# Kernel tuning notes

Measured on AMD Instinct MI355X. Metric: run time of the kernel, lower is better.

Reference implementation:

```python
import jax, jax.numpy as jnp
import numpy as np

N_LEVELS = 1024
K = 8  # number of spike timesteps; d/T have length K+1 (index 0 unused)
X_SHAPE = (64, 512, 1024)


def setup_inputs() -> dict:
    key = jax.random.key(0)
    kx, kh0, kh, kd, kT = jax.random.split(key, 5)
    x = jax.random.normal(kx, X_SHAPE, dtype=jnp.float32) * 2.0
    # h: [N_LEVELS, K+1]; column 0 is the sorted search grid (required by searchsorted)
    h0 = jnp.sort(jax.random.uniform(kh0, (N_LEVELS,), minval=-4.0, maxval=4.0))
    h = jax.random.normal(kh, (N_LEVELS, K + 1), dtype=jnp.float32)
    h = h.at[:, 0].set(h0)
    d = jax.random.uniform(kd, (K + 1,), minval=0.05, maxval=1.0)
    T = jax.random.uniform(kT, (K + 1,), minval=-1.0, maxval=1.0)
    b = jnp.float32(0.1)
    return {"x": x, "h": h, "d": d, "T": T, "b": b}


def reference(x, h, d, T, b):
    sp = x.shape
    xf = x.reshape(-1)
    grid = h[:, 0]  # sorted lookup grid
    n = grid.shape[0]
    idx = jnp.clip(jnp.searchsorted(grid, xf), 1, n - 1)
    left = grid[idx - 1]
    right = grid[idx]
    take_left = jnp.abs(xf - left) < jnp.abs(xf - right)
    nearest = jnp.where(take_left, left, right)          # quantized input
    nidx = jnp.where(take_left, idx - 1, idx)            # per-element row into h
    kmax = d.shape[0] - 1
    v = nearest
    out = jnp.zeros_like(xf)
    # loop over the small fixed number of thresholds (data dims fully vectorized)
    for t in range(1, kmax + 1):
        z = (v - T[t] >= 0).astype(xf.dtype)
        out = out + z * d[t]
        if t != kmax:
            v = h[nidx, t + 1]  # irregular per-element gather
    out = out - b
    return out.reshape(sp)
```

## Files before the change

kernel.cpp:

```cpp
#include <hip/hip_runtime.h>
#include <math.h>

#define NL  1024
#define KP1 9
#define NB  8192

#define WS_TAB 4
#define WS_BS  1028
#define WS_BKT 2060

__device__ __forceinline__ unsigned oi(float f) {
    unsigned u = __float_as_uint(f);
    return (u & 0x80000000u) ? ~u : (u | 0x80000000u);
}
__device__ __forceinline__ float unoi(unsigned k) {
    return __uint_as_float((k & 0x80000000u) ? (k & 0x7fffffffu) : ~k);
}

__device__ __forceinline__ int bidx(float x, float lo0, float inv) {
    float t = (x - lo0) * inv;
    int j = (int)t;
    j = j < 0 ? 0 : j;
    j = j > (NB - 1) ? (NB - 1) : j;
    return j;
}

__global__ __launch_bounds__(1024) void build_kernel(
    const float* __restrict__ h, const float* __restrict__ d,
    const float* __restrict__ T, const float* __restrict__ bp,
    float* __restrict__ ws)
{
    __shared__ float s_g[NL];
    __shared__ float s_B[NL];
    __shared__ int   s_jb[NL];
    __shared__ float s_lo0, s_inv;

    const int tid = threadIdx.x;
    float g = h[tid * KP1];
    s_g[tid] = g;

    {
        float v = g, outv = 0.0f, b = bp[0];
#pragma unroll
        for (int t = 1; t <= 8; ++t) {
            float z = ((v - T[t]) >= 0.0f) ? 1.0f : 0.0f;
            outv = outv + z * d[t];
            if (t != 8) v = h[tid * KP1 + (t + 1)];
        }
        ws[WS_TAB + tid] = outv - b;
    }
    __syncthreads();

    if (tid < NL - 1) {
        float l = s_g[tid], r = s_g[tid + 1];
        unsigned a = oi(l), b2 = oi(r);
        while (a < b2) {
            unsigned m = a + ((b2 - a) >> 1);
            float xm = unoi(m);
            float dl = fabsf(xm - l), dr = fabsf(xm - r);
            if (!(dl < dr)) b2 = m; else a = m + 1;
        }
        s_B[tid] = unoi(a);
    } else {
        s_B[tid] = INFINITY;
    }
    __syncthreads();

    if (tid == 0) {
        float lo0 = s_B[0];
        float inv = (float)NB / (s_B[NL - 2] - lo0);
        s_lo0 = lo0; s_inv = inv;
        ws[0] = lo0; ws[1] = inv;
    }
    __syncthreads();

    float lo0 = s_lo0, inv = s_inv;
    s_jb[tid] = (tid < NL - 1) ? bidx(s_B[tid], lo0, inv) : 0x7fffffff;
    ws[WS_BS + tid] = s_B[tid];
    if (tid < 8) ws[WS_BS + NL + tid] = INFINITY;
    __syncthreads();

    unsigned short* bucket = (unsigned short*)(ws + WS_BKT);
    for (int j = tid; j < NB; j += 1024) {
        int lo = 0;
#pragma unroll
        for (int s = 512; s >= 1; s >>= 1)
            if (s_jb[lo + s - 1] < j) lo += s;
        bucket[j] = (unsigned short)lo;
    }
}

__global__ __launch_bounds__(256) void ps_act_kernel(
    const float* __restrict__ x,
    const float* __restrict__ ws,
    float* __restrict__ out,
    int n4)
{
    __shared__ float          stab[NL];
    __shared__ float          sBs[NL + 8];
    __shared__ unsigned short sbk[NB];

    const int tid = threadIdx.x;
    for (int i = tid; i < NL; i += 256)     stab[i] = ws[WS_TAB + i];
    for (int i = tid; i < NL + 8; i += 256) sBs[i]  = ws[WS_BS + i];
    const unsigned short* gbk = (const unsigned short*)(ws + WS_BKT);
    for (int i = tid; i < NB; i += 256)     sbk[i]  = gbk[i];
    const float lo0 = ws[0];
    const float inv = ws[1];
    __syncthreads();

    const float4* __restrict__ x4 = (const float4*)x;
    float4* __restrict__ o4 = (float4*)out;
    const int stride = gridDim.x * blockDim.x;

    for (int i4 = blockIdx.x * blockDim.x + tid; i4 < n4; i4 += stride) {
        float4 xv = x4[i4];
        float xin[4] = {xv.x, xv.y, xv.z, xv.w};
        float xo[4];
#pragma unroll
        for (int e = 0; e < 4; ++e) {
            float xf = xin[e];
            int j = bidx(xf, lo0, inv);
            int ni = sbk[j];
            while (sBs[ni] <= xf) ++ni;
            xo[e] = stab[ni];
        }
        o4[i4] = make_float4(xo[0], xo[1], xo[2], xo[3]);
    }
}

extern "C" void kernel_launch(void* const* d_in, const int* in_sizes, int n_in,
                              void* d_out, int out_size, void* d_ws, size_t ws_size,
                              hipStream_t stream) {
    const float* x = (const float*)d_in[0];
    const float* h = (const float*)d_in[1];
    const float* d = (const float*)d_in[2];
    const float* T = (const float*)d_in[3];
    const float* b = (const float*)d_in[4];
    float* out = (float*)d_out;
    float* ws  = (float*)d_ws;

    int n  = in_sizes[0];
    int n4 = n / 4;

    build_kernel<<<1, 1024, 0, stream>>>(h, d, T, b, ws);
    ps_act_kernel<<<4096, 256, 0, stream>>>(x, ws, out, n4);
}
```

Measured before the change: 253.8 us.

## Replace bucket index plus linear scan with per-bucket resolved lookup records

The bucket table now stores a float4 record per bucket holding the single boundary and the left and right output values, so most elements resolve with one LDS read and one compare. Buckets with two or more boundaries fall back to a linear scan over global memory. Bucket count drops to 2048 so the records fit in LDS. Loads and stores become nontemporal and the grid shrinks to 1024 blocks. Trade-off: coarser buckets may send more elements down the slower global fallback path, which also diverges.

```diff
diff --git a/kernel.cpp b/kernel.cpp
--- a/kernel.cpp
+++ b/kernel.cpp
@@ -3,11 +3,13 @@
 
 #define NL  1024
 #define KP1 9
-#define NB  8192
+#define NB  2048
 
 #define WS_TAB 4
 #define WS_BS  1028
-#define WS_BKT 2060
+#define WS_REC 2064
+
+typedef float f32x4 __attribute__((ext_vector_type(4)));
 
 __device__ __forceinline__ unsigned oi(float f) {
     unsigned u = __float_as_uint(f);
@@ -32,6 +34,7 @@
 {
     __shared__ float s_g[NL];
     __shared__ float s_B[NL];
+    __shared__ float s_tab[NL];
     __shared__ int   s_jb[NL];
     __shared__ float s_lo0, s_inv;
 
@@ -47,7 +50,9 @@
             outv = outv + z * d[t];
             if (t != 8) v = h[tid * KP1 + (t + 1)];
         }
-        ws[WS_TAB + tid] = outv - b;
+        float tv = outv - b;
+        s_tab[tid] = tv;
+        ws[WS_TAB + tid] = tv;
     }
     __syncthreads();
 
@@ -80,13 +85,22 @@
     if (tid < 8) ws[WS_BS + NL + tid] = INFINITY;
     __syncthreads();
 
-    unsigned short* bucket = (unsigned short*)(ws + WS_BKT);
+    float4* rec = (float4*)(ws + WS_REC);
     for (int j = tid; j < NB; j += 1024) {
-        int lo = 0;
+        int s0 = 0, s1 = 0;
 #pragma unroll
         for (int s = 512; s >= 1; s >>= 1)
-            if (s_jb[lo + s - 1] < j) lo += s;
-        bucket[j] = (unsigned short)lo;
+            if (s_jb[s0 + s - 1] < j) s0 += s;
+#pragma unroll
+        for (int s = 512; s >= 1; s >>= 1)
+            if (s_jb[s1 + s - 1] < j + 1) s1 += s;
+        int cnt = s1 - s0;
+        float S, vL, vR; unsigned aux = 0u;
+        if (cnt == 0)      { S = INFINITY; vL = s_tab[s0]; vR = vL; }
+        else if (cnt == 1) { S = s_B[s0];  vL = s_tab[s0]; vR = s_tab[s0 + 1]; }
+        else               { S = 0.0f; vL = 0.0f; vR = 0.0f;
+                             aux = 0x80000000u | (unsigned)s0; }
+        rec[j] = make_float4(S, vL, vR, __uint_as_float(aux));
     }
 }
 
@@ -96,36 +110,40 @@
     float* __restrict__ out,
     int n4)
 {
-    __shared__ float          stab[NL];
-    __shared__ float          sBs[NL + 8];
-    __shared__ unsigned short sbk[NB];
+    __shared__ float4 srec[NB];
 
     const int tid = threadIdx.x;
-    for (int i = tid; i < NL; i += 256)     stab[i] = ws[WS_TAB + i];
-    for (int i = tid; i < NL + 8; i += 256) sBs[i]  = ws[WS_BS + i];
-    const unsigned short* gbk = (const unsigned short*)(ws + WS_BKT);
-    for (int i = tid; i < NB; i += 256)     sbk[i]  = gbk[i];
+    const float4* grec = (const float4*)(ws + WS_REC);
+    for (int i = tid; i < NB; i += 256) srec[i] = grec[i];
     const float lo0 = ws[0];
     const float inv = ws[1];
+    const float* __restrict__ gB   = ws + WS_BS;
+    const float* __restrict__ gtab = ws + WS_TAB;
     __syncthreads();
 
-    const float4* __restrict__ x4 = (const float4*)x;
-    float4* __restrict__ o4 = (float4*)out;
+    const f32x4* __restrict__ x4 = (const f32x4*)x;
+    f32x4* __restrict__ o4 = (f32x4*)out;
     const int stride = gridDim.x * blockDim.x;
 
     for (int i4 = blockIdx.x * blockDim.x + tid; i4 < n4; i4 += stride) {
-        float4 xv = x4[i4];
-        float xin[4] = {xv.x, xv.y, xv.z, xv.w};
+        f32x4 xv = __builtin_nontemporal_load(&x4[i4]);
         float xo[4];
 #pragma unroll
         for (int e = 0; e < 4; ++e) {
-            float xf = xin[e];
+            float xf = xv[e];
             int j = bidx(xf, lo0, inv);
-            int ni = sbk[j];
-            while (sBs[ni] <= xf) ++ni;
-            xo[e] = stab[ni];
+            float4 q = srec[j];
+            float r = (xf >= q.x) ? q.z : q.y;
+            unsigned a = __float_as_uint(q.w);
+            if (a) {
+                int ni = (int)(a & 0x7fffffffu);
+                while (gB[ni] <= xf) ++ni;
+                r = gtab[ni];
+            }
+            xo[e] = r;
         }
-        o4[i4] = make_float4(xo[0], xo[1], xo[2], xo[3]);
+        f32x4 ov = {xo[0], xo[1], xo[2], xo[3]};
+        __builtin_nontemporal_store(ov, &o4[i4]);
     }
 }
 
@@ -144,5 +162,5 @@
     int n4 = n / 4;
 
     build_kernel<<<1, 1024, 0, stream>>>(h, d, T, b, ws);
-    ps_act_kernel<<<4096, 256, 0, stream>>>(x, ws, out, n4);
+    ps_act_kernel<<<1024, 256, 0, stream>>>(x, ws, out, n4);
 }
```

New measurement: 336.1 us. +32.4%, slower.
